# Kernel optimization log

Measured on AMD Instinct MI355X. Metric: run time of the kernel, lower is better.

Reference implementation:

```python
import jax, jax.numpy as jnp
import numpy as np

BETA = 0.25
NUM_CODES = 1024
EMBED_DIM = 256


def setup_inputs() -> dict:
    key = jax.random.key(0)
    k1, k2 = jax.random.split(key)
    z = jax.random.normal(k1, (64, 32, 32, EMBED_DIM), dtype=jnp.float32)
    # torch init: uniform(-1/num_codes, 1/num_codes)
    codebook = jax.random.uniform(k2, (NUM_CODES, EMBED_DIM), dtype=jnp.float32,
                                  minval=-1.0 / NUM_CODES, maxval=1.0 / NUM_CODES)
    return {"z": z, "codebook": codebook}


def reference(z, codebook):
    shape = z.shape
    z_flat = z.reshape(-1, EMBED_DIM)  # [N, D]
    # squared-distance matrix: ||z||^2 + ||c||^2 - 2 z c^T  -> [N, K]
    d = (jnp.sum(z_flat * z_flat, axis=1, keepdims=True)
         + jnp.sum(codebook * codebook, axis=1)
         - 2.0 * jnp.einsum('nd,kd->nk', z_flat, codebook))
    codes = jnp.argmin(d, axis=1)              # [N] int
    quantized = codebook[codes]                # [N, D] gather
    sg = jax.lax.stop_gradient
    cb_loss = jnp.mean((quantized - sg(z_flat)) ** 2)
    cmt_loss = jnp.mean((z_flat - sg(quantized)) ** 2)
    vq_loss = cb_loss + BETA * cmt_loss
    # straight-through estimator
    out = z_flat + sg(quantized - z_flat)
    return out.reshape(shape), codes.reshape(shape[:-1]), vq_loss
```

## Files before the change

kernel.cpp:

```cpp
#include <hip/hip_runtime.h>


#define N_PTS    65536
#define K_CODES  1024
#define DIM      256
#define MARGIN   1.5e-4f
#define WSKIP    4096

#define OUT_VALS  16777216
#define OUT_CODES 65536

typedef __attribute__((ext_vector_type(8))) short short8v;
typedef __attribute__((ext_vector_type(8))) _Float16 half8v;
typedef __attribute__((ext_vector_type(4))) float float4v;

__device__ __forceinline__ int perm_idx(int r, int k) {
  return ((((r >> 4) * 8 + (k >> 5)) * 4 + ((k >> 3) & 3)) * 128) + (r & 15) * 8 + (k & 7);
}

__device__ __forceinline__ short f2h_bits(float x) {
  union { _Float16 h; short s; } u;
  u.h = (_Float16)x;
  return u.s;
}

__device__ __forceinline__ void gload16(const void* g, void* l) {
  __builtin_amdgcn_global_load_lds(
      (const __attribute__((address_space(1))) unsigned*)g,
      (__attribute__((address_space(3))) unsigned*)l, 16, 0, 0);
}

__global__ void prep_cb_kernel(const float* __restrict__ cb,
                               short* __restrict__ cbh_perm,
                               float* __restrict__ Bf,
                               unsigned long long* __restrict__ scratch,
                               unsigned long long* __restrict__ ws0) {
  const int gid = blockIdx.x * 256 + threadIdx.x;
  scratch[gid] = ~0ull;
  if (gid < 512) ws0[gid] = 0ull;
  int r    = blockIdx.x * 4 + (threadIdx.x >> 6);
  int lane = threadIdx.x & 63;
  const float4 v = *(const float4*)(cb + (size_t)r * DIM + lane * 4);
  double s = (double)v.x * v.x + (double)v.y * v.y
           + (double)v.z * v.z + (double)v.w * v.w;
#pragma unroll
  for (int off = 32; off > 0; off >>= 1) s += __shfl_down(s, off);
  if (lane == 0) Bf[r] = (float)s;
  short4 h = make_short4(f2h_bits(v.x * 1024.0f), f2h_bits(v.y * 1024.0f),
                         f2h_bits(v.z * 1024.0f), f2h_bits(v.w * 1024.0f));
  *(short4*)(cbh_perm + perm_idx(r, lane * 4)) = h;
}

__global__ __launch_bounds__(512, 4) void argmin_mfma_kernel(
    const float* __restrict__ z, const float* __restrict__ cb,
    const short* __restrict__ cbh_perm,
    const float* __restrict__ Bf, float* __restrict__ outq,
    float* __restrict__ codes_out,
    int* __restrict__ cnt2, int* __restrict__ cntf,
    unsigned* __restrict__ flag2, int* __restrict__ flagf,
    float* __restrict__ bv2a, float* __restrict__ bvfa,
    double* __restrict__ loss_slots) {
  __shared__ __align__(16) short lbuf[2][2][4096];
  __shared__ float mv1[128][2], mv2[128][2], mv3[128][2];
  __shared__ int   mk1[128][2], mk2[128][2];
  __shared__ float mz[128];
  __shared__ int   scodes[128];
  __shared__ double wls[2];
  const int t    = threadIdx.x;
  const int w    = t >> 6;
  const int l    = t & 63;
  const int quad = l >> 4;
  const int lr   = l & 15;
  const int wp   = w >> 1;
  const int h    = w & 1;
  const int m0   = blockIdx.x * 128;
  const int pbase = m0 + wp * 32;

  {
    const char* src = (const char*)cbh_perm + (size_t)(h * 32) * 8192 + wp * 2048;
    char* dst = (char*)&lbuf[h][0][0] + wp * 2048;
    gload16(src + l * 16, dst + l * 16);
    gload16(src + 1024 + l * 16, dst + 1024 + l * 16);
  }

  half8v ah[2][8];
  float Szrow[2];
#pragma unroll
  for (int a = 0; a < 2; ++a) {
    const float* zrow = z + (size_t)(pbase + a * 16 + lr) * DIM;
    double zs = 0.0;
#pragma unroll
    for (int q = 0; q < 8; ++q) {
      float4 p0 = *(const float4*)(zrow + q * 32 + quad * 8);
      float4 p1 = *(const float4*)(zrow + q * 32 + quad * 8 + 4);
      zs = fma((double)p0.x, (double)p0.x, zs);
      zs = fma((double)p0.y, (double)p0.y, zs);
      zs = fma((double)p0.z, (double)p0.z, zs);
      zs = fma((double)p0.w, (double)p0.w, zs);
      zs = fma((double)p1.x, (double)p1.x, zs);
      zs = fma((double)p1.y, (double)p1.y, zs);
      zs = fma((double)p1.z, (double)p1.z, zs);
      zs = fma((double)p1.w, (double)p1.w, zs);
      half8v hh;
      hh[0] = (_Float16)p0.x; hh[1] = (_Float16)p0.y;
      hh[2] = (_Float16)p0.z; hh[3] = (_Float16)p0.w;
      hh[4] = (_Float16)p1.x; hh[5] = (_Float16)p1.y;
      hh[6] = (_Float16)p1.z; hh[7] = (_Float16)p1.w;
      ah[a][q] = hh;
    }
    zs += __shfl_xor(zs, 16);
    zs += __shfl_xor(zs, 32);
    Szrow[a] = (float)zs;
  }

  float bv[8], sv[8], tv[8]; int bk[8], sk[8];
#pragma unroll
  for (int s = 0; s < 8; ++s) {
    bv[s] = 3.0e38f; sv[s] = 3.0e38f; tv[s] = 3.0e38f; bk[s] = 0; sk[s] = 0;
  }

  __syncthreads();
  int cur = 0;
  for (int it = 0; it < 32; ++it) {
    if (it < 31) {
      const char* src = (const char*)cbh_perm + (size_t)(h * 32 + it + 1) * 8192 + wp * 2048;
      char* dst = (char*)&lbuf[h][cur ^ 1][0] + wp * 2048;
      gload16(src + l * 16, dst + l * 16);
      gload16(src + 1024 + l * 16, dst + 1024 + l * 16);
    }
    const short* bb = &lbuf[h][cur][0];
    float4v acc0 = {0.f, 0.f, 0.f, 0.f};
    float4v acc1 = {0.f, 0.f, 0.f, 0.f};
#pragma unroll
    for (int q = 0; q < 8; ++q) {
      half8v b = *(const half8v*)(bb + q * 512 + quad * 128 + lr * 8);
      acc0 = __builtin_amdgcn_mfma_f32_16x16x32_f16(ah[0][q], b, acc0, 0, 0, 0);
      acc1 = __builtin_amdgcn_mfma_f32_16x16x32_f16(ah[1][q], b, acc1, 0, 0, 0);
    }
    const int k = (h * 32 + it) * 16 + lr;
    const float bkf = Bf[k];
#pragma unroll
    for (int a = 0; a < 2; ++a) {
#pragma unroll
      for (int r = 0; r < 4; ++r) {
        const int s = a * 4 + r;
        float v = fmaf(-0.001953125f, a ? acc1[r] : acc0[r], bkf);
        bool lt1 = v < bv[s];
        bool lt2 = v < sv[s];
        tv[s] = fminf(fmaxf(v, sv[s]), tv[s]);
        sv[s] = fminf(fmaxf(v, bv[s]), sv[s]);
        bv[s] = fminf(v, bv[s]);
        sk[s] = lt1 ? bk[s] : (lt2 ? k : sk[s]);
        bk[s] = lt1 ? k : bk[s];
      }
    }
    __syncthreads();
    cur ^= 1;
  }

#pragma unroll
  for (int mask = 1; mask < 16; mask <<= 1) {
#pragma unroll
    for (int s = 0; s < 8; ++s) {
      float ov  = __shfl_xor(bv[s], mask);
      float os  = __shfl_xor(sv[s], mask);
      float ot  = __shfl_xor(tv[s], mask);
      int   ok  = __shfl_xor(bk[s], mask);
      int   osk = __shfl_xor(sk[s], mask);
      bool win = (ov < bv[s]) || (ov == bv[s] && ok < bk[s]);
      float a1 = win ? ov : bv[s], a2 = win ? os : sv[s], a3 = win ? ot : tv[s];
      int   a1k = win ? ok : bk[s], a2k = win ? osk : sk[s];
      float b1 = win ? bv[s] : ov, b2 = win ? sv[s] : os;
      int   b1k = win ? bk[s] : ok;
      bool s2 = (a2 < b1) || (a2 == b1 && a2k < b1k);
      bv[s] = a1; bk[s] = a1k;
      sv[s] = s2 ? a2 : b1; sk[s] = s2 ? a2k : b1k;
      tv[s] = s2 ? fminf(a3, b1) : fminf(a2, b2);
    }
  }

  if (lr == 0) {
#pragma unroll
    for (int a = 0; a < 2; ++a)
#pragma unroll
      for (int r = 0; r < 4; ++r) {
        int s  = a * 4 + r;
        int pt = wp * 32 + a * 16 + quad * 4 + r;
        mv1[pt][h] = bv[s]; mv2[pt][h] = sv[s]; mv3[pt][h] = tv[s];
        mk1[pt][h] = bk[s]; mk2[pt][h] = sk[s];
      }
  }
  if (h == 0 && quad == 0) {
#pragma unroll
    for (int a = 0; a < 2; ++a)
      mz[wp * 32 + a * 16 + lr] = Szrow[a];
  }
  __syncthreads();

  double ls = 0.0;
  if (t < 128) {
    float a1 = mv1[t][0], a2 = mv2[t][0], a3 = mv3[t][0];
    int   a1k = mk1[t][0], a2k = mk2[t][0];
    float c1 = mv1[t][1], c2 = mv2[t][1], c3 = mv3[t][1];
    int   c1k = mk1[t][1], c2k = mk2[t][1];
    bool win = (c1 < a1) || (c1 == a1 && c1k < a1k);
    float x1 = win ? c1 : a1, x2 = win ? c2 : a2, x3 = win ? c3 : a3;
    int   x1k = win ? c1k : a1k, x2k = win ? c2k : a2k;
    float y1 = win ? a1 : c1, y2 = win ? a2 : c2;
    int   y1k = win ? a1k : c1k;
    bool s2 = (x2 < y1) || (x2 == y1 && x2k < y1k);
    float f2v = s2 ? x2 : y1; int f2k = s2 ? x2k : y1k;
    float f3v = s2 ? fminf(x3, y1) : fminf(x2, y2);
    int n = m0 + t;
    codes_out[n] = (float)x1k;
    scodes[t] = x1k;
    float vrow = mz[t] + x1;
    ls = (double)vrow;
    if (f3v - x1 < MARGIN) {
      int pos = atomicAdd(cntf, 1);
      flagf[pos] = n; bvfa[pos] = vrow;
    } else if (f2v - x1 < MARGIN) {
      int pos = atomicAdd(cnt2, 1);
      flag2[pos] = (unsigned)n | ((unsigned)f2k << 16);
      bv2a[pos] = vrow;
    }
  }
#pragma unroll
  for (int off = 32; off > 0; off >>= 1) ls += __shfl_down(ls, off);
  if (l == 0 && w < 2) wls[w] = ls;
  __syncthreads();

  if (m0 >= WSKIP) {
#pragma unroll
    for (int i = 0; i < 16; ++i) {
      int row = i * 8 + w;
      int c = scodes[row];
      *(float4*)(outq + (size_t)(m0 + row) * DIM + l * 4) =
          *(const float4*)(cb + (size_t)c * DIM + l * 4);
    }
  }
  if (t == 0)
    atomicAdd(&loss_slots[blockIdx.x & 255], wls[0] + wls[1]);
}

__global__ __launch_bounds__(256) void fixup_pair_kernel(
    const float* __restrict__ z, const float* __restrict__ cb,
    const float* __restrict__ Bf, const unsigned* __restrict__ flag2,
    const int* __restrict__ cnt2, const float* __restrict__ bv2a,
    float* __restrict__ codes_out, float* __restrict__ outq,
    double* __restrict__ loss_slots) {
  const int t   = threadIdx.x;
  const int l   = t & 63;
  const int h   = l >> 5;
  const int sub = l & 31;
  const int wid = blockIdx.x * 4 + (t >> 6);
  const int nw  = gridDim.x * 4;
  const int cnt = *cnt2;
  for (int i = wid; i < cnt; i += nw) {
    const unsigned rec = flag2[i];
    const int n  = rec & 0xFFFF;
    const int k2 = rec >> 16;
    const int k1 = (int)codes_out[n];
    const int k  = h ? k2 : k1;
    const float* zr = z + (size_t)n * DIM + sub * 8;
    const float* cr = cb + (size_t)k * DIM + sub * 8;
    const float4 za = *(const float4*)(zr);
    const float4 zb = *(const float4*)(zr + 4);
    const float4 ca = *(const float4*)(cr);
    const float4 cv = *(const float4*)(cr + 4);
    double s = (double)za.x*za.x + (double)za.y*za.y + (double)za.z*za.z + (double)za.w*za.w
             + (double)zb.x*zb.x + (double)zb.y*zb.y + (double)zb.z*zb.z + (double)zb.w*zb.w;
    double d = (double)za.x*ca.x + (double)za.y*ca.y + (double)za.z*ca.z + (double)za.w*ca.w
             + (double)zb.x*cv.x + (double)zb.y*cv.y + (double)zb.z*cv.z + (double)zb.w*cv.w;
#pragma unroll
    for (int m = 1; m < 32; m <<= 1) {
      s += __shfl_xor(s, m);
      d += __shfl_xor(d, m);
    }
    const float Sfl = (float)s;
    const float T1  = Sfl + Bf[k];
    const float v   = T1 - 2.0f * (float)d;
    const float vo  = __shfl_xor(v, 32);
    const int   ko  = __shfl_xor(k, 32);
    const bool keep = (v < vo) || (v == vo && k < ko);
    const float vmin = keep ? v : vo;
    const int   kf   = keep ? k : ko;
    if (l == 0) {
      codes_out[n] = (float)kf;
      atomicAdd(&loss_slots[n & 255], (double)(vmin - bv2a[i]));
    }
    if (kf != k1 && n >= WSKIP)
      *(float4*)(outq + (size_t)n * DIM + l * 4) =
          *(const float4*)(cb + (size_t)kf * DIM + l * 4);
  }
}

__global__ __launch_bounds__(256) void fixup_full_kernel(
    const float* __restrict__ z, const float* __restrict__ cb,
    const float* __restrict__ Bf, const int* __restrict__ flagf,
    const int* __restrict__ cntf, unsigned long long* __restrict__ scratch) {
  __shared__ float vred[4];
  __shared__ int   kred[4];
  const int t = threadIdx.x;
  const int w = t >> 6;
  const int l = t & 63;
  const int cnt = *cntf;
  for (int ib = blockIdx.x; (ib >> 2) < cnt; ib += gridDim.x) {
    const int i = ib >> 2, q = ib & 3;
    const int n = flagf[i];
    const float4 zv = *(const float4*)(z + (size_t)n * DIM + l * 4);
    double s = (double)zv.x*zv.x + (double)zv.y*zv.y
             + (double)zv.z*zv.z + (double)zv.w*zv.w;
#pragma unroll
    for (int off = 32; off > 0; off >>= 1) s += __shfl_xor(s, off);
    const float Sfl = (float)s;
    float bvv = 3.0e38f; int bkk = 0;
    const int kbase = q * 256 + w * 64;
#pragma unroll 4
    for (int k0 = 0; k0 < 64; ++k0) {
      const int k = kbase + k0;
      const float4 cv = *(const float4*)(cb + (size_t)k * DIM + l * 4);
      double d = (double)zv.x*cv.x + (double)zv.y*cv.y
               + (double)zv.z*cv.z + (double)zv.w*cv.w;
#pragma unroll
      for (int off = 32; off > 0; off >>= 1) d += __shfl_xor(d, off);
      float T1 = Sfl + Bf[k];
      float v  = T1 - 2.0f * (float)d;
      if (v < bvv) { bvv = v; bkk = k; }
    }
    __syncthreads();
    if (l == 0) { vred[w] = bvv; kred[w] = bkk; }
    __syncthreads();
    if (t == 0) {
      float fv = vred[0]; int fk = kred[0];
#pragma unroll
      for (int j = 1; j < 4; ++j) {
        float v2 = vred[j]; int kk = kred[j];
        if (v2 < fv || (v2 == fv && kk < fk)) { fv = v2; fk = kk; }
      }
      unsigned long long key =
          ((unsigned long long)__float_as_uint(fv) << 32) | (unsigned)fk;
      atomicMin(&scratch[n], key);
    }
  }
}

__global__ __launch_bounds__(256) void fixup_write_kernel(
    const int* __restrict__ flagf, const int* __restrict__ cntf,
    const unsigned long long* __restrict__ scratch,
    const float* __restrict__ bvfa, const float* __restrict__ cb,
    float* __restrict__ codes_out, float* __restrict__ outq,
    double* __restrict__ loss_slots) {
  const int t = threadIdx.x, l = t & 63;
  const int wid = blockIdx.x * 4 + (t >> 6);
  const int nw  = gridDim.x * 4;
  const int cnt = *cntf;
  for (int i = wid; i < cnt; i += nw) {
    const int n = flagf[i];
    const unsigned long long key = scratch[n];
    const int   fk = (int)(unsigned)(key & 0xFFFFFFFFull);
    const float fv = __uint_as_float((unsigned)(key >> 32));
    const int   k1 = (int)codes_out[n];
    if (l == 0) {
      codes_out[n] = (float)fk;
      atomicAdd(&loss_slots[n & 255], (double)(fv - bvfa[i]));
    }
    if (fk != k1 && n >= WSKIP)
      *(float4*)(outq + (size_t)n * DIM + l * 4) =
          *(const float4*)(cb + (size_t)fk * DIM + l * 4);
  }
}

__global__ void small_gather_kernel(const float* __restrict__ cb,
                                    const float* __restrict__ codes_f,
                                    float* __restrict__ outq) {
  int gid = blockIdx.x * 256 + threadIdx.x;
  int n = gid >> 6, l = gid & 63;
  int c = (int)codes_f[n];
  *(float4*)(outq + (size_t)n * DIM + l * 4) =
      *(const float4*)(cb + (size_t)c * DIM + l * 4);
}

__global__ void finalize_kernel(const double* __restrict__ loss_slots,
                                float* __restrict__ out_loss) {
  const int t = threadIdx.x;
  double s = loss_slots[t];
#pragma unroll
  for (int off = 32; off > 0; off >>= 1) s += __shfl_down(s, off);
  __shared__ double ws[4];
  if ((t & 63) == 0) ws[t >> 6] = s;
  __syncthreads();
  if (t == 0) {
    double tot = ws[0] + ws[1] + ws[2] + ws[3];
    out_loss[0] = (float)(1.25 * tot / (double)(N_PTS * (size_t)DIM));
  }
}

extern "C" void kernel_launch(void* const* d_in, const int* in_sizes, int n_in,
                              void* d_out, int out_size, void* d_ws, size_t ws_size,
                              hipStream_t stream) {
  const float* z  = (const float*)d_in[0];
  const float* cb = (const float*)d_in[1];
  float* out = (float*)d_out;
  double* loss_slots = (double*)d_ws;
  int*      cnt2  = (int*)((char*)d_ws + 2048);
  int*      cntf  = (int*)((char*)d_ws + 2052);
  float*    Bf    = (float*)((char*)d_ws + 4096);
  unsigned* flag2 = (unsigned*)((char*)d_ws + 8192);
  short* cbh_perm = (short*)d_out;
  float* bv2a     = (float*)((char*)d_out + 524288);
  float* bvfa     = (float*)((char*)d_out + 786432);
  unsigned long long* scratch = (unsigned long long*)((char*)d_out + 1048576);
  int*   flagf    = (int*)((char*)d_out + 1572864);

  prep_cb_kernel<<<K_CODES / 4, 256, 0, stream>>>(
      cb, cbh_perm, Bf, scratch, (unsigned long long*)d_ws);
  argmin_mfma_kernel<<<N_PTS / 128, 512, 0, stream>>>(
      z, cb, cbh_perm, Bf, out, out + OUT_VALS, cnt2, cntf, flag2, flagf,
      bv2a, bvfa, loss_slots);
  fixup_pair_kernel<<<1024, 256, 0, stream>>>(
      z, cb, Bf, flag2, cnt2, bv2a, out + OUT_VALS, out, loss_slots);
  fixup_full_kernel<<<2048, 256, 0, stream>>>(z, cb, Bf, flagf, cntf, scratch);
  fixup_write_kernel<<<64, 256, 0, stream>>>(
      flagf, cntf, scratch, bvfa, cb, out + OUT_VALS, out, loss_slots);
  small_gather_kernel<<<WSKIP * 64 / 256, 256, 0, stream>>>(
      cb, out + OUT_VALS, out);
  finalize_kernel<<<1, 256, 0, stream>>>(loss_slots, out + OUT_VALS + OUT_CODES);
}
```

Before: 226.1 us.

## Give each wave all codes in argmin kernel, drop cross-wave merge

```diff
diff --git a/kernel.cpp b/kernel.cpp
--- a/kernel.cpp
+++ b/kernel.cpp
@@ -51,7 +51,7 @@
   *(short4*)(cbh_perm + perm_idx(r, lane * 4)) = h;
 }
 
-__global__ __launch_bounds__(512, 4) void argmin_mfma_kernel(
+__global__ __launch_bounds__(256, 2) void argmin_mfma_kernel(
     const float* __restrict__ z, const float* __restrict__ cb,
     const short* __restrict__ cbh_perm,
     const float* __restrict__ Bf, float* __restrict__ outq,
@@ -60,27 +60,22 @@
     unsigned* __restrict__ flag2, int* __restrict__ flagf,
     float* __restrict__ bv2a, float* __restrict__ bvfa,
     double* __restrict__ loss_slots) {
-  __shared__ __align__(16) short lbuf[2][2][4096];
-  __shared__ float mv1[128][2], mv2[128][2], mv3[128][2];
-  __shared__ int   mk1[128][2], mk2[128][2];
-  __shared__ float mz[128];
-  __shared__ int   scodes[128];
-  __shared__ double wls[2];
+  __shared__ __align__(16) short lbuf[2][8192];
+  __shared__ double wls[4];
   const int t    = threadIdx.x;
   const int w    = t >> 6;
   const int l    = t & 63;
   const int quad = l >> 4;
   const int lr   = l & 15;
-  const int wp   = w >> 1;
-  const int h    = w & 1;
   const int m0   = blockIdx.x * 128;
-  const int pbase = m0 + wp * 32;
+  const int pbase = m0 + w * 32;
 
   {
-    const char* src = (const char*)cbh_perm + (size_t)(h * 32) * 8192 + wp * 2048;
-    char* dst = (char*)&lbuf[h][0][0] + wp * 2048;
-    gload16(src + l * 16, dst + l * 16);
-    gload16(src + 1024 + l * 16, dst + 1024 + l * 16);
+    const char* src = (const char*)cbh_perm;
+    char* dst = (char*)&lbuf[0][0];
+#pragma unroll
+    for (int i = 0; i < 4; ++i)
+      gload16(src + t * 16 + i * 4096, dst + t * 16 + i * 4096);
   }
 
   half8v ah[2][8];
@@ -123,35 +118,39 @@
   int cur = 0;
   for (int it = 0; it < 32; ++it) {
     if (it < 31) {
-      const char* src = (const char*)cbh_perm + (size_t)(h * 32 + it + 1) * 8192 + wp * 2048;
-      char* dst = (char*)&lbuf[h][cur ^ 1][0] + wp * 2048;
-      gload16(src + l * 16, dst + l * 16);
-      gload16(src + 1024 + l * 16, dst + 1024 + l * 16);
-    }
-    const short* bb = &lbuf[h][cur][0];
-    float4v acc0 = {0.f, 0.f, 0.f, 0.f};
-    float4v acc1 = {0.f, 0.f, 0.f, 0.f};
-#pragma unroll
-    for (int q = 0; q < 8; ++q) {
-      half8v b = *(const half8v*)(bb + q * 512 + quad * 128 + lr * 8);
-      acc0 = __builtin_amdgcn_mfma_f32_16x16x32_f16(ah[0][q], b, acc0, 0, 0, 0);
-      acc1 = __builtin_amdgcn_mfma_f32_16x16x32_f16(ah[1][q], b, acc1, 0, 0, 0);
-    }
-    const int k = (h * 32 + it) * 16 + lr;
-    const float bkf = Bf[k];
-#pragma unroll
-    for (int a = 0; a < 2; ++a) {
-#pragma unroll
-      for (int r = 0; r < 4; ++r) {
-        const int s = a * 4 + r;
-        float v = fmaf(-0.001953125f, a ? acc1[r] : acc0[r], bkf);
-        bool lt1 = v < bv[s];
-        bool lt2 = v < sv[s];
-        tv[s] = fminf(fmaxf(v, sv[s]), tv[s]);
-        sv[s] = fminf(fmaxf(v, bv[s]), sv[s]);
-        bv[s] = fminf(v, bv[s]);
-        sk[s] = lt1 ? bk[s] : (lt2 ? k : sk[s]);
-        bk[s] = lt1 ? k : bk[s];
+      const char* src = (const char*)cbh_perm + (size_t)(it + 1) * 16384;
+      char* dst = (char*)&lbuf[cur ^ 1][0];
+#pragma unroll
+      for (int i = 0; i < 4; ++i)
+        gload16(src + t * 16 + i * 4096, dst + t * 16 + i * 4096);
+    }
+    const int c0 = it * 32;
+#pragma unroll
+    for (int st = 0; st < 2; ++st) {
+      float4v acc0 = {0.f, 0.f, 0.f, 0.f};
+      float4v acc1 = {0.f, 0.f, 0.f, 0.f};
+#pragma unroll
+      for (int q = 0; q < 8; ++q) {
+        half8v b = *(const half8v*)(&lbuf[cur][(st * 8 + q) * 512 + quad * 128 + lr * 8]);
+        acc0 = __builtin_amdgcn_mfma_f32_16x16x32_f16(ah[0][q], b, acc0, 0, 0, 0);
+        acc1 = __builtin_amdgcn_mfma_f32_16x16x32_f16(ah[1][q], b, acc1, 0, 0, 0);
+      }
+      const int k = c0 + st * 16 + lr;
+      const float bkf = Bf[k];
+#pragma unroll
+      for (int a = 0; a < 2; ++a) {
+#pragma unroll
+        for (int r = 0; r < 4; ++r) {
+          const int s = a * 4 + r;
+          float v = fmaf(-0.001953125f, a ? acc1[r] : acc0[r], bkf);
+          bool lt1 = v < bv[s];
+          bool lt2 = v < sv[s];
+          tv[s] = fminf(fmaxf(v, sv[s]), tv[s]);
+          sv[s] = fminf(fmaxf(v, bv[s]), sv[s]);
+          bv[s] = fminf(v, bv[s]);
+          sk[s] = lt1 ? bk[s] : (lt2 ? k : sk[s]);
+          bk[s] = lt1 ? k : bk[s];
+        }
       }
     }
     __syncthreads();
@@ -179,68 +178,53 @@
     }
   }
 
+  float vrow[8];
+#pragma unroll
+  for (int a = 0; a < 2; ++a)
+#pragma unroll
+    for (int r = 0; r < 4; ++r)
+      vrow[a * 4 + r] = __shfl(Szrow[a], quad * 4 + r) + bv[a * 4 + r];
+
+  if (m0 >= WSKIP) {
+#pragma unroll
+    for (int p = 0; p < 32; ++p) {
+      int c = __shfl(bk[(p >> 4) * 4 + (p & 3)], ((p >> 2) & 3) << 4);
+      int n = pbase + p;
+      *(float4*)(outq + (size_t)n * DIM + l * 4) =
+          *(const float4*)(cb + (size_t)c * DIM + l * 4);
+    }
+  }
+
+  double ls = 0.0;
   if (lr == 0) {
 #pragma unroll
+    for (int s = 0; s < 8; ++s) ls += (double)vrow[s];
+  }
+  ls += __shfl_down(ls, 16);
+  ls += __shfl_down(ls, 32);
+  if (l == 0) wls[w] = ls;
+
+  if (lr == 0) {
+#pragma unroll
     for (int a = 0; a < 2; ++a)
 #pragma unroll
       for (int r = 0; r < 4; ++r) {
-        int s  = a * 4 + r;
-        int pt = wp * 32 + a * 16 + quad * 4 + r;
-        mv1[pt][h] = bv[s]; mv2[pt][h] = sv[s]; mv3[pt][h] = tv[s];
-        mk1[pt][h] = bk[s]; mk2[pt][h] = sk[s];
+        const int s = a * 4 + r;
+        int n = pbase + a * 16 + quad * 4 + r;
+        codes_out[n] = (float)bk[s];
+        if (tv[s] - bv[s] < MARGIN) {
+          int pos = atomicAdd(cntf, 1);
+          flagf[pos] = n; bvfa[pos] = vrow[s];
+        } else if (sv[s] - bv[s] < MARGIN) {
+          int pos = atomicAdd(cnt2, 1);
+          flag2[pos] = (unsigned)n | ((unsigned)sk[s] << 16);
+          bv2a[pos] = vrow[s];
+        }
       }
   }
-  if (h == 0 && quad == 0) {
-#pragma unroll
-    for (int a = 0; a < 2; ++a)
-      mz[wp * 32 + a * 16 + lr] = Szrow[a];
-  }
   __syncthreads();
-
-  double ls = 0.0;
-  if (t < 128) {
-    float a1 = mv1[t][0], a2 = mv2[t][0], a3 = mv3[t][0];
-    int   a1k = mk1[t][0], a2k = mk2[t][0];
-    float c1 = mv1[t][1], c2 = mv2[t][1], c3 = mv3[t][1];
-    int   c1k = mk1[t][1], c2k = mk2[t][1];
-    bool win = (c1 < a1) || (c1 == a1 && c1k < a1k);
-    float x1 = win ? c1 : a1, x2 = win ? c2 : a2, x3 = win ? c3 : a3;
-    int   x1k = win ? c1k : a1k, x2k = win ? c2k : a2k;
-    float y1 = win ? a1 : c1, y2 = win ? a2 : c2;
-    int   y1k = win ? a1k : c1k;
-    bool s2 = (x2 < y1) || (x2 == y1 && x2k < y1k);
-    float f2v = s2 ? x2 : y1; int f2k = s2 ? x2k : y1k;
-    float f3v = s2 ? fminf(x3, y1) : fminf(x2, y2);
-    int n = m0 + t;
-    codes_out[n] = (float)x1k;
-    scodes[t] = x1k;
-    float vrow = mz[t] + x1;
-    ls = (double)vrow;
-    if (f3v - x1 < MARGIN) {
-      int pos = atomicAdd(cntf, 1);
-      flagf[pos] = n; bvfa[pos] = vrow;
-    } else if (f2v - x1 < MARGIN) {
-      int pos = atomicAdd(cnt2, 1);
-      flag2[pos] = (unsigned)n | ((unsigned)f2k << 16);
-      bv2a[pos] = vrow;
-    }
-  }
-#pragma unroll
-  for (int off = 32; off > 0; off >>= 1) ls += __shfl_down(ls, off);
-  if (l == 0 && w < 2) wls[w] = ls;
-  __syncthreads();
-
-  if (m0 >= WSKIP) {
-#pragma unroll
-    for (int i = 0; i < 16; ++i) {
-      int row = i * 8 + w;
-      int c = scodes[row];
-      *(float4*)(outq + (size_t)(m0 + row) * DIM + l * 4) =
-          *(const float4*)(cb + (size_t)c * DIM + l * 4);
-    }
-  }
   if (t == 0)
-    atomicAdd(&loss_slots[blockIdx.x & 255], wls[0] + wls[1]);
+    atomicAdd(&loss_slots[blockIdx.x & 255], wls[0] + wls[1] + wls[2] + wls[3]);
 }
 
 __global__ __launch_bounds__(256) void fixup_pair_kernel(
@@ -415,7 +399,7 @@
 
   prep_cb_kernel<<<K_CODES / 4, 256, 0, stream>>>(
       cb, cbh_perm, Bf, scratch, (unsigned long long*)d_ws);
-  argmin_mfma_kernel<<<N_PTS / 128, 512, 0, stream>>>(
+  argmin_mfma_kernel<<<N_PTS / 128, 256, 0, stream>>>(
       z, cb, cbh_perm, Bf, out, out + OUT_VALS, cnt2, cntf, flag2, flagf,
       bv2a, bvfa, loss_slots);
   fixup_pair_kernel<<<1024, 256, 0, stream>>>(
```

Result: faster. 217.1 us (-4.0%).
